# Optimization experiments

Hardware: AMD Instinct MI355X
Metric: run time of the kernel (lower is better)

Reference implementation:

```python
import jax, jax.numpy as jnp
import numpy as np

E, H, I = 8, 2048, 4096      # experts, hidden, intermediate
T, K = 1024, 2               # tokens, top_k
GS = 128                     # quantization group size


def setup_inputs() -> dict:
    key = jax.random.key(0)
    ks = jax.random.split(key, 9)
    x = jax.random.normal(ks[0], (T, H), dtype=jnp.float32)
    # packed int4: two nibbles per uint8, [out_features, in_features // 2]
    gu_packed = jax.random.randint(ks[1], (E, 2 * I, H // 2), 0, 256, dtype=jnp.int32).astype(jnp.uint8)
    dn_packed = jax.random.randint(ks[2], (E, H, I // 2), 0, 256, dtype=jnp.int32).astype(jnp.uint8)
    # small positive scales; zeros chosen so dequantized values center near 0
    gu_scales = jax.random.uniform(ks[3], (E, 2 * I, H // GS), dtype=jnp.float32) * 0.02 + 0.001
    gu_zeros = -7.5 * gu_scales + 0.001 * jax.random.normal(ks[4], gu_scales.shape, dtype=jnp.float32)
    dn_scales = jax.random.uniform(ks[5], (E, H, I // GS), dtype=jnp.float32) * 0.02 + 0.001
    dn_zeros = -7.5 * dn_scales + 0.001 * jax.random.normal(ks[6], dn_scales.shape, dtype=jnp.float32)
    router_indices = jax.random.randint(ks[7], (T, K), 0, E, dtype=jnp.int32)
    rw = jax.random.uniform(ks[8], (T, K), dtype=jnp.float32) + 0.1
    routing_weights = rw / jnp.sum(rw, axis=-1, keepdims=True)
    return {
        "x": x,
        "gu_packed": gu_packed, "gu_scales": gu_scales, "gu_zeros": gu_zeros,
        "dn_packed": dn_packed, "dn_scales": dn_scales, "dn_zeros": dn_zeros,
        "router_indices": router_indices, "routing_weights": routing_weights,
        "group_size": GS,
    }


def _dequantize_packed_weight(packed, scales, zeros, in_features, group_size):
    """Unpack uint8 nibbles (high at even cols, low at odd cols), apply
    per-group scale and zero-point: w = q * scale + zero."""
    out_f = packed.shape[0]
    high = (packed >> 4) & 15
    low = packed & 15
    # interleave: column 0::2 = high nibble, 1::2 = low nibble
    unpacked = jnp.stack([high, low], axis=-1).reshape(out_f, -1).astype(scales.dtype)
    n_groups = scales.shape[1]
    grouped = unpacked.reshape(out_f, n_groups, group_size)
    dq = grouped * scales[:, :, None] + zeros[:, :, None]
    return dq.reshape(out_f, n_groups * group_size)[:, :in_features]


def reference(x, gu_packed, gu_scales, gu_zeros, dn_packed, dn_scales, dn_zeros,
              router_indices, routing_weights, group_size):
    num_experts = gu_packed.shape[0]
    hidden = x.shape[-1]
    inter = dn_packed.shape[2] * 2
    # per-token per-expert combine coefficient [T, E]
    one_hot = jax.nn.one_hot(router_indices, num_experts, dtype=x.dtype)  # [T, K, E]
    coef = jnp.einsum("tke,tk->te", one_hot, routing_weights)
    out = jnp.zeros_like(x)
    for e in range(num_experts):
        gu_w = _dequantize_packed_weight(gu_packed[e], gu_scales[e], gu_zeros[e], hidden, group_size)  # [2I, H]
        dn_w = _dequantize_packed_weight(dn_packed[e], dn_scales[e], dn_zeros[e], inter, group_size)   # [H, I]
        gu = x @ gu_w.T                     # [T, 2I]
        gate, up = jnp.split(gu, 2, axis=-1)
        h = jax.nn.gelu(gate, approximate=True) * up  # [T, I]
        out = out + coef[:, e:e + 1] * (h @ dn_w.T)   # [T, H]
    return out
```

## Files before the change

kernel.cpp:

```cpp
#include <hip/hip_runtime.h>
#include <stdint.h>

#define E_ 8
#define H_ 2048
#define I_ 4096
#define T_ 1024
#define K_ 2
#define GS_ 128
#define NPAIR (T_ * K_)

#define BM 128
#define BN 64
#define BK 64

#define CH(r, c) ((((c) ^ ((r) & 7)) << 3))

typedef __attribute__((ext_vector_type(8))) short s16x8;
typedef _Float16 f16x2 __attribute__((ext_vector_type(2)));
typedef _Float16 f16x8 __attribute__((ext_vector_type(8)));
typedef __attribute__((ext_vector_type(4))) float f32x4;

static __device__ __forceinline__ unsigned short f2h(float f) {
    _Float16 h = (_Float16)f;
    return __builtin_bit_cast(unsigned short, h);
}
static __device__ __forceinline__ uint32_t pkrtz(float lo, float hi) {
    return __builtin_bit_cast(uint32_t, __builtin_amdgcn_cvt_pkrtz(lo, hi));
}

__global__ void x2h_kernel(const float* __restrict__ x, unsigned short* __restrict__ xh) {
    int i = (blockIdx.x * 256 + threadIdx.x) * 8;
    float4 a = *(const float4*)(x + i);
    float4 b = *(const float4*)(x + i + 4);
    uint4 st = make_uint4(pkrtz(a.x, a.y), pkrtz(a.z, a.w),
                          pkrtz(b.x, b.y), pkrtz(b.z, b.w));
    *(uint4*)(xh + i) = st;
}

__global__ void zero_f4(float4* p, int n4) {
    int i = blockIdx.x * blockDim.x + threadIdx.x;
    if (i < n4) p[i] = make_float4(0.f, 0.f, 0.f, 0.f);
}

__global__ void router_kernel(const int* __restrict__ ridx,
                              const float* __restrict__ rw,
                              int* __restrict__ seg,
                              int* __restrict__ ptok,
                              float* __restrict__ pw)
{
    __shared__ int cnt[E_];
    __shared__ int cur[E_];
    int tid = threadIdx.x;
    if (tid < E_) cnt[tid] = 0;
    __syncthreads();
    for (int p = tid; p < NPAIR; p += blockDim.x)
        atomicAdd(&cnt[ridx[p]], 1);
    __syncthreads();
    if (tid == 0) {
        int s = 0;
        for (int e = 0; e < E_; e++) { seg[e] = s; cur[e] = s; s += cnt[e]; }
        seg[E_] = s;
    }
    __syncthreads();
    for (int p = tid; p < NPAIR; p += blockDim.x) {
        int e = ridx[p];
        int pos = atomicAdd(&cur[e], 1);
        ptok[pos] = p >> 1;
        pw[pos] = rw[p];
    }
}

static __device__ __forceinline__ void dq_chunk(int4 q, f16x2 sc, f16x2 zp,
                                                unsigned short* dst) {
    uint32_t r[4];
    int qa[4] = {q.x, q.y, q.z, q.w};
    const f16x2 k1024 = {(_Float16)1024.f, (_Float16)1024.f};
#pragma unroll
    for (int j = 0; j < 4; j++) {
        uint32_t b = (uint32_t)qa[j];
        uint32_t p = 0x64006400u | (b >> 4) | ((b & 0xfu) << 16);
        f16x2 ph = __builtin_bit_cast(f16x2, p);
        f16x2 w = (ph - k1024) * sc + zp;
        r[j] = __builtin_bit_cast(uint32_t, w);
    }
    *(uint4*)dst = make_uint4(r[0], r[1], r[2], r[3]);
}

__global__ __launch_bounds__(256, 3) void gemm1_kernel(
    const unsigned short* __restrict__ xh,
    const int* __restrict__ gu_packed,
    const float* __restrict__ gu_scales,
    const float* __restrict__ gu_zeros,
    const int* __restrict__ seg,
    const int* __restrict__ ptok,
    unsigned short* __restrict__ h_act)
{
    const int e = blockIdx.z;
    const int seg0 = seg[e], seg1 = seg[e + 1];
    const int m0 = blockIdx.y * BM;
    if (seg0 + m0 >= seg1) return;
    const int n0 = blockIdx.x * BN;

    __shared__ __align__(16) unsigned short sX[BM * 64];
    __shared__ __align__(16) unsigned short sG[BN * 64];
    __shared__ __align__(16) unsigned short sU[BN * 64];

    const int tid = threadIdx.x;
    const int lane = tid & 63;
    const int wave = tid >> 6;
    const int wm = (wave >> 1) * 64;
    const int wn = (wave & 1) * 32;
    const int quad = lane >> 4;
    const int l16 = lane & 15;

    const int xr = tid >> 1;
    const int xc0 = (tid & 1) * 4;
    int slotX = seg0 + m0 + xr;
    if (slotX > NPAIR - 1) slotX = NPAIR - 1;
    const unsigned short* xrow = xh + (size_t)ptok[slotX] * H_ + xc0 * 8;

    const int wr = tid >> 2;
    const int wc0 = (tid & 3) * 2;
    const int ng = n0 + wr;
    const int nu = n0 + I_ + wr;
    const int* gprow = gu_packed + ((size_t)e * (2 * I_) + ng) * (H_ / 2) + (tid & 3) * 8;
    const int* uprow = gu_packed + ((size_t)e * (2 * I_) + nu) * (H_ / 2) + (tid & 3) * 8;
    const float* gsrow = gu_scales + ((size_t)e * (2 * I_) + ng) * (H_ / GS_);
    const float* gzrow = gu_zeros  + ((size_t)e * (2 * I_) + ng) * (H_ / GS_);
    const float* usrow = gu_scales + ((size_t)e * (2 * I_) + nu) * (H_ / GS_);
    const float* uzrow = gu_zeros  + ((size_t)e * (2 * I_) + nu) * (H_ / GS_);

    f32x4 accg[4][2], accu[4][2];
#pragma unroll
    for (int mi = 0; mi < 4; mi++)
#pragma unroll
        for (int ni = 0; ni < 2; ni++) {
            accg[mi][ni] = (f32x4){0.f, 0.f, 0.f, 0.f};
            accu[mi][ni] = (f32x4){0.f, 0.f, 0.f, 0.f};
        }

    s16x8 rX[4];
    int4 rG[2], rU[2];
    float rgs, rgz, rus, ruz;

    {
        const s16x8* xp = (const s16x8*)(xrow);
        rX[0] = xp[0]; rX[1] = xp[1]; rX[2] = xp[2]; rX[3] = xp[3];
        const int4* gp = (const int4*)(gprow);
        rG[0] = gp[0]; rG[1] = gp[1];
        const int4* up = (const int4*)(uprow);
        rU[0] = up[0]; rU[1] = up[1];
        rgs = gsrow[0]; rgz = gzrow[0]; rus = usrow[0]; ruz = uzrow[0];
    }

    for (int k0 = 0; k0 < H_; k0 += BK) {
        *(s16x8*)&sX[(xr << 6) + CH(xr, xc0 + 0)] = rX[0];
        *(s16x8*)&sX[(xr << 6) + CH(xr, xc0 + 1)] = rX[1];
        *(s16x8*)&sX[(xr << 6) + CH(xr, xc0 + 2)] = rX[2];
        *(s16x8*)&sX[(xr << 6) + CH(xr, xc0 + 3)] = rX[3];
        {
            f16x2 gs2 = {(_Float16)rgs, (_Float16)rgs};
            f16x2 gz2 = {(_Float16)rgz, (_Float16)rgz};
            f16x2 us2 = {(_Float16)rus, (_Float16)rus};
            f16x2 uz2 = {(_Float16)ruz, (_Float16)ruz};
            dq_chunk(rG[0], gs2, gz2, &sG[(wr << 6) + CH(wr, wc0)]);
            dq_chunk(rG[1], gs2, gz2, &sG[(wr << 6) + CH(wr, wc0 + 1)]);
            dq_chunk(rU[0], us2, uz2, &sU[(wr << 6) + CH(wr, wc0)]);
            dq_chunk(rU[1], us2, uz2, &sU[(wr << 6) + CH(wr, wc0 + 1)]);
        }
        __syncthreads();

        if (k0 + BK < H_) {
            const int k1 = k0 + BK;
            const s16x8* xp = (const s16x8*)(xrow + k1);
            rX[0] = xp[0]; rX[1] = xp[1]; rX[2] = xp[2]; rX[3] = xp[3];
            const int4* gp = (const int4*)(gprow + (k1 >> 1));
            rG[0] = gp[0]; rG[1] = gp[1];
            const int4* up = (const int4*)(uprow + (k1 >> 1));
            rU[0] = up[0]; rU[1] = up[1];
            const int g = k1 >> 7;
            rgs = gsrow[g]; rgz = gzrow[g]; rus = usrow[g]; ruz = uzrow[g];
        }

#pragma unroll
        for (int ks = 0; ks < 2; ks++) {
            const int cb = ks * 4 + quad;
            f16x8 af[4], gf[2], uf[2];
#pragma unroll
            for (int i = 0; i < 4; i++) {
                const int r = wm + i * 16 + l16;
                af[i] = *(const f16x8*)&sX[(r << 6) + CH(r, cb)];
            }
#pragma unroll
            for (int i = 0; i < 2; i++) {
                const int r = wn + i * 16 + l16;
                gf[i] = *(const f16x8*)&sG[(r << 6) + CH(r, cb)];
                uf[i] = *(const f16x8*)&sU[(r << 6) + CH(r, cb)];
            }
#pragma unroll
            for (int mi = 0; mi < 4; mi++)
#pragma unroll
                for (int ni = 0; ni < 2; ni++) {
                    accg[mi][ni] = __builtin_amdgcn_mfma_f32_16x16x32_f16(af[mi], gf[ni], accg[mi][ni], 0, 0, 0);
                    accu[mi][ni] = __builtin_amdgcn_mfma_f32_16x16x32_f16(af[mi], uf[ni], accu[mi][ni], 0, 0, 0);
                }
        }
        __syncthreads();
    }

#pragma unroll
    for (int mi = 0; mi < 4; mi++) {
#pragma unroll
        for (int rr = 0; rr < 4; rr++) {
            const int row = wm + mi * 16 + quad * 4 + rr;
            const int slot = seg0 + m0 + row;
            if (slot < seg1) {
#pragma unroll
                for (int ni = 0; ni < 2; ni++) {
                    const int col = n0 + wn + ni * 16 + l16;
                    float gv = accg[mi][ni][rr];
                    float uv = accu[mi][ni][rr];
                    float t = tanhf(0.7978845608028654f * (gv + 0.044715f * gv * gv * gv));
                    float hv = 0.5f * gv * (1.0f + t) * uv;
                    h_act[(size_t)slot * I_ + col] = f2h(hv);
                }
            }
        }
    }
}

__global__ __launch_bounds__(256, 3) void gemm2_kernel(
    const unsigned short* __restrict__ h_act,
    const int* __restrict__ dn_packed,
    const float* __restrict__ dn_scales,
    const float* __restrict__ dn_zeros,
    const int* __restrict__ seg,
    const int* __restrict__ ptok,
    const float* __restrict__ pw,
    float* __restrict__ out)
{
    const int e = blockIdx.z;
    const int seg0 = seg[e], seg1 = seg[e + 1];
    const int m0 = blockIdx.y * BM;
    if (seg0 + m0 >= seg1) return;
    const int n0 = blockIdx.x * BN;

    __shared__ __align__(16) unsigned short sA[BM * 64];
    __shared__ __align__(16) unsigned short sW[BN * 64];

    const int tid = threadIdx.x;
    const int lane = tid & 63;
    const int wave = tid >> 6;
    const int wm = (wave >> 1) * 64;
    const int wn = (wave & 1) * 32;
    const int quad = lane >> 4;
    const int l16 = lane & 15;

    const int ar = tid >> 1;
    const int ac0 = (tid & 1) * 4;
    int slotA = seg0 + m0 + ar;
    if (slotA > NPAIR - 1) slotA = NPAIR - 1;
    const unsigned short* arow = h_act + (size_t)slotA * I_ + ac0 * 8;

    const int wr = tid >> 2;
    const int wc0 = (tid & 3) * 2;
    const int nw = n0 + wr;
    const int* wprow = dn_packed + ((size_t)e * H_ + nw) * (I_ / 2) + (tid & 3) * 8;
    const float* wsrow = dn_scales + ((size_t)e * H_ + nw) * (I_ / GS_);
    const float* wzrow = dn_zeros  + ((size_t)e * H_ + nw) * (I_ / GS_);

    f32x4 acc[4][2];
#pragma unroll
    for (int mi = 0; mi < 4; mi++)
#pragma unroll
        for (int ni = 0; ni < 2; ni++)
            acc[mi][ni] = (f32x4){0.f, 0.f, 0.f, 0.f};

    s16x8 rA[4];
    int4 rW[2];
    float rs, rz;

    {
        const s16x8* ap = (const s16x8*)(arow);
        rA[0] = ap[0]; rA[1] = ap[1]; rA[2] = ap[2]; rA[3] = ap[3];
        const int4* wp = (const int4*)(wprow);
        rW[0] = wp[0]; rW[1] = wp[1];
        rs = wsrow[0]; rz = wzrow[0];
    }

    for (int k0 = 0; k0 < I_; k0 += BK) {
        *(s16x8*)&sA[(ar << 6) + CH(ar, ac0 + 0)] = rA[0];
        *(s16x8*)&sA[(ar << 6) + CH(ar, ac0 + 1)] = rA[1];
        *(s16x8*)&sA[(ar << 6) + CH(ar, ac0 + 2)] = rA[2];
        *(s16x8*)&sA[(ar << 6) + CH(ar, ac0 + 3)] = rA[3];
        {
            f16x2 ws2 = {(_Float16)rs, (_Float16)rs};
            f16x2 wz2 = {(_Float16)rz, (_Float16)rz};
            dq_chunk(rW[0], ws2, wz2, &sW[(wr << 6) + CH(wr, wc0)]);
            dq_chunk(rW[1], ws2, wz2, &sW[(wr << 6) + CH(wr, wc0 + 1)]);
        }
        __syncthreads();

        if (k0 + BK < I_) {
            const int k1 = k0 + BK;
            const s16x8* ap = (const s16x8*)(arow + k1);
            rA[0] = ap[0]; rA[1] = ap[1]; rA[2] = ap[2]; rA[3] = ap[3];
            const int4* wp = (const int4*)(wprow + (k1 >> 1));
            rW[0] = wp[0]; rW[1] = wp[1];
            const int g = k1 >> 7;
            rs = wsrow[g]; rz = wzrow[g];
        }

#pragma unroll
        for (int ks = 0; ks < 2; ks++) {
            const int cb = ks * 4 + quad;
            f16x8 af[4], wf[2];
#pragma unroll
            for (int i = 0; i < 4; i++) {
                const int r = wm + i * 16 + l16;
                af[i] = *(const f16x8*)&sA[(r << 6) + CH(r, cb)];
            }
#pragma unroll
            for (int i = 0; i < 2; i++) {
                const int r = wn + i * 16 + l16;
                wf[i] = *(const f16x8*)&sW[(r << 6) + CH(r, cb)];
            }
#pragma unroll
            for (int mi = 0; mi < 4; mi++)
#pragma unroll
                for (int ni = 0; ni < 2; ni++)
                    acc[mi][ni] = __builtin_amdgcn_mfma_f32_16x16x32_f16(af[mi], wf[ni], acc[mi][ni], 0, 0, 0);
        }
        __syncthreads();
    }

#pragma unroll
    for (int mi = 0; mi < 4; mi++) {
#pragma unroll
        for (int rr = 0; rr < 4; rr++) {
            const int row = wm + mi * 16 + quad * 4 + rr;
            const int slot = seg0 + m0 + row;
            if (slot < seg1) {
                const int tok = ptok[slot];
                const float cf = pw[slot];
#pragma unroll
                for (int ni = 0; ni < 2; ni++) {
                    const int col = n0 + wn + ni * 16 + l16;
                    atomicAdd(&out[(size_t)tok * H_ + col], cf * acc[mi][ni][rr]);
                }
            }
        }
    }
}

extern "C" void kernel_launch(void* const* d_in, const int* in_sizes, int n_in,
                              void* d_out, int out_size, void* d_ws, size_t ws_size,
                              hipStream_t stream) {
    const float* x    = (const float*)d_in[0];
    const int*   gu_p = (const int*)d_in[1];
    const float* gu_s = (const float*)d_in[2];
    const float* gu_z = (const float*)d_in[3];
    const int*   dn_p = (const int*)d_in[4];
    const float* dn_s = (const float*)d_in[5];
    const float* dn_z = (const float*)d_in[6];
    const int*   ridx = (const int*)d_in[7];
    const float* rw   = (const float*)d_in[8];

    char* ws = (char*)d_ws;
    int*            seg   = (int*)ws;
    int*            ptok  = (int*)(ws + 256);
    float*          pw    = (float*)(ws + 256 + NPAIR * 4);
    unsigned short* h_act = (unsigned short*)(ws + 32768);
    unsigned short* xh    = (unsigned short*)(ws + 32768 + (size_t)NPAIR * I_ * 2);

    float* out = (float*)d_out;

    x2h_kernel<<<T_ * H_ / (256 * 8), 256, 0, stream>>>(x, xh);
    zero_f4<<<(T_ * H_ / 4 + 255) / 256, 256, 0, stream>>>((float4*)out, T_ * H_ / 4);
    router_kernel<<<1, 256, 0, stream>>>(ridx, rw, seg, ptok, pw);
    gemm1_kernel<<<dim3(I_ / BN, NPAIR / BM, E_), 256, 0, stream>>>(
        xh, gu_p, gu_s, gu_z, seg, ptok, h_act);
    gemm2_kernel<<<dim3(H_ / BN, NPAIR / BM, E_), 256, 0, stream>>>(
        h_act, dn_p, dn_s, dn_z, seg, ptok, pw, out);
}
```

Before: 680.8 us.

## Load tiles straight to LDS and dequantize int4 weights at fragment read

Both expert GEMM kernels now use global_load_lds to copy activation and packed weight tiles directly from global memory into LDS, removing the register staging and LDS store pass. Weights stay packed in LDS, shrinking the weight tile footprint. Each wave dequantizes its own MFMA fragments right after reading them, with scales and zeros loaded per lane per tile. In exchange, the register-prefetch overlap of the next tile with current compute is gone. Waves that share the same columns also repeat the dequantization work.

```diff
diff --git a/kernel.cpp b/kernel.cpp
--- a/kernel.cpp
+++ b/kernel.cpp
@@ -13,12 +13,13 @@
 #define BN 64
 #define BK 64
 
-#define CH(r, c) ((((c) ^ ((r) & 7)) << 3))
-
-typedef __attribute__((ext_vector_type(8))) short s16x8;
+#define CH(r, c)  ((((c) ^ ((r) & 7)) << 3))
+#define CHI(r, c) ((((c) ^ ((r) & 7)) << 2))
+
 typedef _Float16 f16x2 __attribute__((ext_vector_type(2)));
 typedef _Float16 f16x8 __attribute__((ext_vector_type(8)));
 typedef __attribute__((ext_vector_type(4))) float f32x4;
+typedef uint32_t u32x4 __attribute__((ext_vector_type(4)));
 
 static __device__ __forceinline__ unsigned short f2h(float f) {
     _Float16 h = (_Float16)f;
@@ -26,6 +27,11 @@
 }
 static __device__ __forceinline__ uint32_t pkrtz(float lo, float hi) {
     return __builtin_bit_cast(uint32_t, __builtin_amdgcn_cvt_pkrtz(lo, hi));
+}
+static __device__ __forceinline__ void gload_lds16(const void* g, void* l) {
+    __builtin_amdgcn_global_load_lds(
+        (const __attribute__((address_space(1))) void*)g,
+        (__attribute__((address_space(3))) void*)l, 16, 0, 0);
 }
 
 __global__ void x2h_kernel(const float* __restrict__ x, unsigned short* __restrict__ xh) {
@@ -70,20 +76,22 @@
     }
 }
 
-static __device__ __forceinline__ void dq_chunk(int4 q, f16x2 sc, f16x2 zp,
-                                                unsigned short* dst) {
-    uint32_t r[4];
+static __device__ __forceinline__ f16x8 dq_frag(int4 q, float sc, float zp) {
+    f16x2 s2 = {(_Float16)sc, (_Float16)sc};
+    f16x2 z2 = {(_Float16)zp, (_Float16)zp};
+    const f16x2 k1024 = {(_Float16)1024.f, (_Float16)1024.f};
+    uint32_t rr[4];
     int qa[4] = {q.x, q.y, q.z, q.w};
-    const f16x2 k1024 = {(_Float16)1024.f, (_Float16)1024.f};
 #pragma unroll
     for (int j = 0; j < 4; j++) {
         uint32_t b = (uint32_t)qa[j];
         uint32_t p = 0x64006400u | (b >> 4) | ((b & 0xfu) << 16);
         f16x2 ph = __builtin_bit_cast(f16x2, p);
-        f16x2 w = (ph - k1024) * sc + zp;
-        r[j] = __builtin_bit_cast(uint32_t, w);
-    }
-    *(uint4*)dst = make_uint4(r[0], r[1], r[2], r[3]);
+        f16x2 w = (ph - k1024) * s2 + z2;
+        rr[j] = __builtin_bit_cast(uint32_t, w);
+    }
+    u32x4 v = {rr[0], rr[1], rr[2], rr[3]};
+    return __builtin_bit_cast(f16x8, v);
 }
 
 __global__ __launch_bounds__(256, 3) void gemm1_kernel(
@@ -102,8 +110,8 @@
     const int n0 = blockIdx.x * BN;
 
     __shared__ __align__(16) unsigned short sX[BM * 64];
-    __shared__ __align__(16) unsigned short sG[BN * 64];
-    __shared__ __align__(16) unsigned short sU[BN * 64];
+    __shared__ __align__(16) int sG[BN * 32];
+    __shared__ __align__(16) int sU[BN * 32];
 
     const int tid = threadIdx.x;
     const int lane = tid & 63;
@@ -113,22 +121,31 @@
     const int quad = lane >> 4;
     const int l16 = lane & 15;
 
-    const int xr = tid >> 1;
-    const int xc0 = (tid & 1) * 4;
-    int slotX = seg0 + m0 + xr;
-    if (slotX > NPAIR - 1) slotX = NPAIR - 1;
-    const unsigned short* xrow = xh + (size_t)ptok[slotX] * H_ + xc0 * 8;
-
-    const int wr = tid >> 2;
-    const int wc0 = (tid & 3) * 2;
-    const int ng = n0 + wr;
-    const int nu = n0 + I_ + wr;
-    const int* gprow = gu_packed + ((size_t)e * (2 * I_) + ng) * (H_ / 2) + (tid & 3) * 8;
-    const int* uprow = gu_packed + ((size_t)e * (2 * I_) + nu) * (H_ / 2) + (tid & 3) * 8;
-    const float* gsrow = gu_scales + ((size_t)e * (2 * I_) + ng) * (H_ / GS_);
-    const float* gzrow = gu_zeros  + ((size_t)e * (2 * I_) + ng) * (H_ / GS_);
-    const float* usrow = gu_scales + ((size_t)e * (2 * I_) + nu) * (H_ / GS_);
-    const float* uzrow = gu_zeros  + ((size_t)e * (2 * I_) + nu) * (H_ / GS_);
+    const int lr = lane >> 3;
+    const int lc = (lane & 7) ^ lr;
+
+    const unsigned short* xp[4];
+#pragma unroll
+    for (int i = 0; i < 4; i++) {
+        int r = (wave * 4 + i) * 8 + lr;
+        int slot = seg0 + m0 + r;
+        if (slot > NPAIR - 1) slot = NPAIR - 1;
+        xp[i] = xh + (size_t)ptok[slot] * H_ + lc * 8;
+    }
+    const int* gpG[2];
+    const int* gpU[2];
+#pragma unroll
+    for (int i = 0; i < 2; i++) {
+        int r = (wave * 2 + i) * 8 + lr;
+        gpG[i] = gu_packed + ((size_t)e * (2 * I_) + n0 + r) * (H_ / 2) + lc * 4;
+        gpU[i] = gu_packed + ((size_t)e * (2 * I_) + I_ + n0 + r) * (H_ / 2) + lc * 4;
+    }
+    const int NGRP = H_ / GS_;
+    int bi[2];
+#pragma unroll
+    for (int i = 0; i < 2; i++)
+        bi[i] = ((e * 2 * I_) + n0 + wn + i * 16 + l16) * NGRP;
+    const int uoff = I_ * NGRP;
 
     f32x4 accg[4][2], accu[4][2];
 #pragma unroll
@@ -139,48 +156,28 @@
             accu[mi][ni] = (f32x4){0.f, 0.f, 0.f, 0.f};
         }
 
-    s16x8 rX[4];
-    int4 rG[2], rU[2];
-    float rgs, rgz, rus, ruz;
-
-    {
-        const s16x8* xp = (const s16x8*)(xrow);
-        rX[0] = xp[0]; rX[1] = xp[1]; rX[2] = xp[2]; rX[3] = xp[3];
-        const int4* gp = (const int4*)(gprow);
-        rG[0] = gp[0]; rG[1] = gp[1];
-        const int4* up = (const int4*)(uprow);
-        rU[0] = up[0]; rU[1] = up[1];
-        rgs = gsrow[0]; rgz = gzrow[0]; rus = usrow[0]; ruz = uzrow[0];
-    }
-
-    for (int k0 = 0; k0 < H_; k0 += BK) {
-        *(s16x8*)&sX[(xr << 6) + CH(xr, xc0 + 0)] = rX[0];
-        *(s16x8*)&sX[(xr << 6) + CH(xr, xc0 + 1)] = rX[1];
-        *(s16x8*)&sX[(xr << 6) + CH(xr, xc0 + 2)] = rX[2];
-        *(s16x8*)&sX[(xr << 6) + CH(xr, xc0 + 3)] = rX[3];
-        {
-            f16x2 gs2 = {(_Float16)rgs, (_Float16)rgs};
-            f16x2 gz2 = {(_Float16)rgz, (_Float16)rgz};
-            f16x2 us2 = {(_Float16)rus, (_Float16)rus};
-            f16x2 uz2 = {(_Float16)ruz, (_Float16)ruz};
-            dq_chunk(rG[0], gs2, gz2, &sG[(wr << 6) + CH(wr, wc0)]);
-            dq_chunk(rG[1], gs2, gz2, &sG[(wr << 6) + CH(wr, wc0 + 1)]);
-            dq_chunk(rU[0], us2, uz2, &sU[(wr << 6) + CH(wr, wc0)]);
-            dq_chunk(rU[1], us2, uz2, &sU[(wr << 6) + CH(wr, wc0 + 1)]);
+    const int NT = H_ / BK;
+    for (int t = 0; t < NT; t++) {
+        const int kx = t * 64;
+        const int kw = t * 32;
+#pragma unroll
+        for (int i = 0; i < 4; i++)
+            gload_lds16(xp[i] + kx, &sX[(wave * 4 + i) * 512]);
+#pragma unroll
+        for (int i = 0; i < 2; i++) {
+            gload_lds16(gpG[i] + kw, &sG[(wave * 2 + i) * 256]);
+            gload_lds16(gpU[i] + kw, &sU[(wave * 2 + i) * 256]);
+        }
+        const int g = t >> 1;
+        float gsv[2], gzv[2], usv[2], uzv[2];
+#pragma unroll
+        for (int i = 0; i < 2; i++) {
+            gsv[i] = gu_scales[bi[i] + g];
+            gzv[i] = gu_zeros [bi[i] + g];
+            usv[i] = gu_scales[bi[i] + uoff + g];
+            uzv[i] = gu_zeros [bi[i] + uoff + g];
         }
         __syncthreads();
-
-        if (k0 + BK < H_) {
-            const int k1 = k0 + BK;
-            const s16x8* xp = (const s16x8*)(xrow + k1);
-            rX[0] = xp[0]; rX[1] = xp[1]; rX[2] = xp[2]; rX[3] = xp[3];
-            const int4* gp = (const int4*)(gprow + (k1 >> 1));
-            rG[0] = gp[0]; rG[1] = gp[1];
-            const int4* up = (const int4*)(uprow + (k1 >> 1));
-            rU[0] = up[0]; rU[1] = up[1];
-            const int g = k1 >> 7;
-            rgs = gsrow[g]; rgz = gzrow[g]; rus = usrow[g]; ruz = uzrow[g];
-        }
 
 #pragma unroll
         for (int ks = 0; ks < 2; ks++) {
@@ -194,8 +191,10 @@
 #pragma unroll
             for (int i = 0; i < 2; i++) {
                 const int r = wn + i * 16 + l16;
-                gf[i] = *(const f16x8*)&sG[(r << 6) + CH(r, cb)];
-                uf[i] = *(const f16x8*)&sU[(r << 6) + CH(r, cb)];
+                int4 qg = *(const int4*)&sG[(r << 5) + CHI(r, cb)];
+                int4 qu = *(const int4*)&sU[(r << 5) + CHI(r, cb)];
+                gf[i] = dq_frag(qg, gsv[i], gzv[i]);
+                uf[i] = dq_frag(qu, usv[i], uzv[i]);
             }
 #pragma unroll
             for (int mi = 0; mi < 4; mi++)
@@ -246,7 +245,7 @@
     const int n0 = blockIdx.x * BN;
 
     __shared__ __align__(16) unsigned short sA[BM * 64];
-    __shared__ __align__(16) unsigned short sW[BN * 64];
+    __shared__ __align__(16) int sW[BN * 32];
 
     const int tid = threadIdx.x;
     const int lane = tid & 63;
@@ -256,18 +255,28 @@
     const int quad = lane >> 4;
     const int l16 = lane & 15;
 
-    const int ar = tid >> 1;
-    const int ac0 = (tid & 1) * 4;
-    int slotA = seg0 + m0 + ar;
-    if (slotA > NPAIR - 1) slotA = NPAIR - 1;
-    const unsigned short* arow = h_act + (size_t)slotA * I_ + ac0 * 8;
-
-    const int wr = tid >> 2;
-    const int wc0 = (tid & 3) * 2;
-    const int nw = n0 + wr;
-    const int* wprow = dn_packed + ((size_t)e * H_ + nw) * (I_ / 2) + (tid & 3) * 8;
-    const float* wsrow = dn_scales + ((size_t)e * H_ + nw) * (I_ / GS_);
-    const float* wzrow = dn_zeros  + ((size_t)e * H_ + nw) * (I_ / GS_);
+    const int lr = lane >> 3;
+    const int lc = (lane & 7) ^ lr;
+
+    const unsigned short* ap[4];
+#pragma unroll
+    for (int i = 0; i < 4; i++) {
+        int r = (wave * 4 + i) * 8 + lr;
+        int slot = seg0 + m0 + r;
+        if (slot > NPAIR - 1) slot = NPAIR - 1;
+        ap[i] = h_act + (size_t)slot * I_ + lc * 8;
+    }
+    const int* wp[2];
+#pragma unroll
+    for (int i = 0; i < 2; i++) {
+        int r = (wave * 2 + i) * 8 + lr;
+        wp[i] = dn_packed + ((size_t)e * H_ + n0 + r) * (I_ / 2) + lc * 4;
+    }
+    const int NGRP = I_ / GS_;
+    int bi[2];
+#pragma unroll
+    for (int i = 0; i < 2; i++)
+        bi[i] = ((e * H_) + n0 + wn + i * 16 + l16) * NGRP;
 
     f32x4 acc[4][2];
 #pragma unroll
@@ -276,40 +285,24 @@
         for (int ni = 0; ni < 2; ni++)
             acc[mi][ni] = (f32x4){0.f, 0.f, 0.f, 0.f};
 
-    s16x8 rA[4];
-    int4 rW[2];
-    float rs, rz;
-
-    {
-        const s16x8* ap = (const s16x8*)(arow);
-        rA[0] = ap[0]; rA[1] = ap[1]; rA[2] = ap[2]; rA[3] = ap[3];
-        const int4* wp = (const int4*)(wprow);
-        rW[0] = wp[0]; rW[1] = wp[1];
-        rs = wsrow[0]; rz = wzrow[0];
-    }
-
-    for (int k0 = 0; k0 < I_; k0 += BK) {
-        *(s16x8*)&sA[(ar << 6) + CH(ar, ac0 + 0)] = rA[0];
-        *(s16x8*)&sA[(ar << 6) + CH(ar, ac0 + 1)] = rA[1];
-        *(s16x8*)&sA[(ar << 6) + CH(ar, ac0 + 2)] = rA[2];
-        *(s16x8*)&sA[(ar << 6) + CH(ar, ac0 + 3)] = rA[3];
-        {
-            f16x2 ws2 = {(_Float16)rs, (_Float16)rs};
-            f16x2 wz2 = {(_Float16)rz, (_Float16)rz};
-            dq_chunk(rW[0], ws2, wz2, &sW[(wr << 6) + CH(wr, wc0)]);
-            dq_chunk(rW[1], ws2, wz2, &sW[(wr << 6) + CH(wr, wc0 + 1)]);
+    const int NT = I_ / BK;
+    for (int t = 0; t < NT; t++) {
+        const int kx = t * 64;
+        const int kw = t * 32;
+#pragma unroll
+        for (int i = 0; i < 4; i++)
+            gload_lds16(ap[i] + kx, &sA[(wave * 4 + i) * 512]);
+#pragma unroll
+        for (int i = 0; i < 2; i++)
+            gload_lds16(wp[i] + kw, &sW[(wave * 2 + i) * 256]);
+        const int g = t >> 1;
+        float sv[2], zv[2];
+#pragma unroll
+        for (int i = 0; i < 2; i++) {
+            sv[i] = dn_scales[bi[i] + g];
+            zv[i] = dn_zeros [bi[i] + g];
         }
         __syncthreads();
-
-        if (k0 + BK < I_) {
-            const int k1 = k0 + BK;
-            const s16x8* ap = (const s16x8*)(arow + k1);
-            rA[0] = ap[0]; rA[1] = ap[1]; rA[2] = ap[2]; rA[3] = ap[3];
-            const int4* wp = (const int4*)(wprow + (k1 >> 1));
-            rW[0] = wp[0]; rW[1] = wp[1];
-            const int g = k1 >> 7;
-            rs = wsrow[g]; rz = wzrow[g];
-        }
 
 #pragma unroll
         for (int ks = 0; ks < 2; ks++) {
@@ -323,7 +316,8 @@
 #pragma unroll
             for (int i = 0; i < 2; i++) {
                 const int r = wn + i * 16 + l16;
-                wf[i] = *(const f16x8*)&sW[(r << 6) + CH(r, cb)];
+                int4 qw = *(const int4*)&sW[(r << 5) + CHI(r, cb)];
+                wf[i] = dq_frag(qw, sv[i], zv[i]);
             }
 #pragma unroll
             for (int mi = 0; mi < 4; mi++)
```

Measured after the change: 861.4 us. 26.5% more time.
